# Performance work log

Measured on AMD Instinct MI355X. Metric: run time of the kernel, lower is better.

## Reference

```python
import jax, jax.numpy as jnp
import numpy as np

N_NODES = 100000


def gcn_layer(x, edge_index, W, b):
    # GCNConv: out = D^{-1/2} (A + I) D^{-1/2} (x W) + b
    N = x.shape[0]
    loop = jnp.arange(N, dtype=edge_index.dtype)
    src = jnp.concatenate([edge_index[0], loop])
    dst = jnp.concatenate([edge_index[1], loop])
    deg = jax.ops.segment_sum(jnp.ones_like(src, dtype=x.dtype), dst, num_segments=N)
    dinv = jnp.where(deg > 0, jax.lax.rsqrt(deg), 0.0)
    norm = dinv[src] * dinv[dst]  # [E+N]
    h = x @ W  # [N, out]
    msg = h[src] * norm[:, None]  # [E+N, out]
    out = jax.ops.segment_sum(msg, dst, num_segments=N)
    return out + b


def setup_inputs() -> dict:
    key = jax.random.key(0)
    ks = jax.random.split(key, 8)
    x = jax.random.normal(ks[0], (N_NODES, 128), dtype=jnp.float32)
    edge_index = jax.random.randint(ks[1], (2, 1600000), 0, N_NODES, dtype=jnp.int32)
    def glorot(k, fan_in, fan_out):
        s = jnp.sqrt(6.0 / (fan_in + fan_out)).astype(jnp.float32)
        return jax.random.uniform(k, (fan_in, fan_out), jnp.float32, -s, s)
    return {
        "x": x,
        "edge_index": edge_index,
        "W1": glorot(ks[2], 128, 64), "b1": jnp.zeros((64,), jnp.float32),
        "W2": glorot(ks[3], 64, 128), "b2": jnp.zeros((128,), jnp.float32),
        "W3": glorot(ks[4], 128, 64), "b3": jnp.zeros((64,), jnp.float32),
    }


def reference(x, edge_index, W1, b1, W2, b2, W3, b3):
    h = jax.nn.relu(gcn_layer(x, edge_index, W1, b1))
    h = jax.nn.relu(gcn_layer(h, edge_index, W2, b2))
    out = gcn_layer(h, edge_index, W3, b3)
    return out
```

## Files before the change

kernel.cpp:

```cpp
#include <hip/hip_runtime.h>
#include <hip/hip_fp16.h>
#include <stdint.h>


#define NWGA 256
#define CMAX 8

struct __align__(8) Half4 { __half x, y, z, w; };

__device__ __forceinline__ float4 fma4(float a, float4 b, float4 c) {
  return make_float4(fmaf(a, b.x, c.x), fmaf(a, b.y, c.y),
                     fmaf(a, b.z, c.z), fmaf(a, b.w, c.w));
}

__global__ __launch_bounds__(256) void bucket_hist_kernel(
    const int* __restrict__ dst, int E, int chunk, int NBUK,
    int* __restrict__ M ) {
  __shared__ int hist[512];
  const int w = blockIdx.x, t = threadIdx.x;
  for (int i = t; i < NBUK; i += 256) hist[i] = 0;
  __syncthreads();
  const int e0 = w * chunk;
  const int e1 = min(e0 + chunk, E);
  for (int e = e0 + t; e < e1; e += 256) atomicAdd(&hist[dst[e] >> 8], 1);
  __syncthreads();
  for (int i = t; i < NBUK; i += 256) M[i * NWGA + w] = hist[i];
}

__global__ void scan_blocksum(const int* __restrict__ data, int len,
                              int* __restrict__ bsum) {
  __shared__ int s[256];
  int i = blockIdx.x * 256 + threadIdx.x;
  s[threadIdx.x] = (i < len) ? data[i] : 0;
  __syncthreads();
  for (int off = 128; off > 0; off >>= 1) {
    if (threadIdx.x < off) s[threadIdx.x] += s[threadIdx.x + off];
    __syncthreads();
  }
  if (threadIdx.x == 0) bsum[blockIdx.x] = s[0];
}

__global__ void scan_bsums(int* bsum, int NB) {
  __shared__ int s[512];
  int t = threadIdx.x;
  int v = (t < NB) ? bsum[t] : 0;
  s[t] = v;
  __syncthreads();
  for (int off = 1; off < 512; off <<= 1) {
    int u = (t >= off) ? s[t - off] : 0;
    __syncthreads();
    s[t] += u;
    __syncthreads();
  }
  if (t < NB) bsum[t] = s[t] - v;
}

__global__ void scan_final(int* __restrict__ data, int len,
                           const int* __restrict__ bsum) {
  __shared__ int s[256];
  int t = threadIdx.x;
  int i = blockIdx.x * 256 + t;
  int v = (i < len) ? data[i] : 0;
  s[t] = v;
  __syncthreads();
  for (int off = 1; off < 256; off <<= 1) {
    int u = (t >= off) ? s[t - off] : 0;
    __syncthreads();
    s[t] += u;
    __syncthreads();
  }
  if (i < len) data[i] = bsum[blockIdx.x] + s[t] - v;
}

__global__ __launch_bounds__(256) void bucket_scatter_kernel(
    const int* __restrict__ ei, int E, int chunk, int NBUK,
    const int* __restrict__ Mscan, int2* __restrict__ edata1) {
  __shared__ int cur[512];
  const int w = blockIdx.x, t = threadIdx.x;
  for (int i = t; i < NBUK; i += 256) cur[i] = Mscan[i * NWGA + w];
  __syncthreads();
  const int e0 = w * chunk;
  const int e1 = min(e0 + chunk, E);
  for (int e = e0 + t; e < e1; e += 256) {
    int s = ei[e];
    int d = ei[E + e];
    int pos = atomicAdd(&cur[d >> 8], 1);
    edata1[pos] = make_int2(s, d);
  }
}

__global__ __launch_bounds__(256) void bucket_sort_kernel(
    const int2* __restrict__ edata1, const int* __restrict__ Mscan, int E,
    int N, int NBUK, int* __restrict__ offsets, float* __restrict__ dinv,
    int* __restrict__ edata2) {
  __shared__ int hist[256];
  __shared__ int cursor[256];
  const int b = blockIdx.x, t = threadIdx.x;
  const int ebase = Mscan[b * NWGA];
  const int eend = (b + 1 < NBUK) ? Mscan[(b + 1) * NWGA] : E;
  const int nodebase = b << 8;
  const int node = nodebase + t;
  const int base = ebase + min(nodebase, N);
  hist[t] = (node < N) ? 1 : 0;
  __syncthreads();
  for (int e = ebase + t; e < eend; e += 256)
    atomicAdd(&hist[edata1[e].y - nodebase], 1);
  __syncthreads();
  const int deg = hist[t];
  for (int off = 1; off < 256; off <<= 1) {
    int u = (t >= off) ? hist[t - off] : 0;
    __syncthreads();
    hist[t] += u;
    __syncthreads();
  }
  const int excl = hist[t] - deg;
  cursor[t] = base + excl + 1;
  if (node < N) {
    offsets[node] = base + excl;
    dinv[node] = rsqrtf((float)deg);
    edata2[base + excl] = node;
  }
  if (node == N - 1) offsets[N] = E + N;
  __syncthreads();
  for (int e = ebase + t; e < eend; e += 256) {
    int2 sd = edata1[e];
    int pos = atomicAdd(&cursor[sd.y - nodebase], 1);
    edata2[pos] = sd.x;
  }
}

__global__ __launch_bounds__(256) void edge_weight_kernel(
    const int* __restrict__ edata2, int EN, int* __restrict__ ed3) {
  int stride = gridDim.x * blockDim.x;
  for (int e = blockIdx.x * blockDim.x + threadIdx.x; e < EN; e += stride)
    ed3[e] = edata2[e] << 7;
}

template <int K, int D, bool BR, bool DSCALE, typename InT, typename OutT>
__global__ __launch_bounds__(256) void gemm_kernel(
    const InT* __restrict__ X, const float* __restrict__ W,
    const float* __restrict__ bias, const float* __restrict__ dinv,
    OutT* __restrict__ H, int N) {
  constexpr int CG = D / 4;
  constexpr int TY = 256 / CG;
  constexpr int ROWS = TY * 4;
  __shared__ float Ws[K * D];
  for (int i = threadIdx.x; i < K * D / 4; i += 256)
    reinterpret_cast<float4*>(Ws)[i] = reinterpret_cast<const float4*>(W)[i];
  __syncthreads();

  const int tx = threadIdx.x % CG;
  const int ty = threadIdx.x / CG;
  const int rbase = blockIdx.x * ROWS + ty;

  float4 acc[4];
  int r[4];
#pragma unroll
  for (int i = 0; i < 4; i++) {
    acc[i] = make_float4(0.f, 0.f, 0.f, 0.f);
    int rr = rbase + i * TY;
    r[i] = (rr < N) ? rr : (N - 1);
  }

  for (int k = 0; k < K; k += 4) {
    float4 wv0 = *reinterpret_cast<const float4*>(&Ws[(k + 0) * D + tx * 4]);
    float4 wv1 = *reinterpret_cast<const float4*>(&Ws[(k + 1) * D + tx * 4]);
    float4 wv2 = *reinterpret_cast<const float4*>(&Ws[(k + 2) * D + tx * 4]);
    float4 wv3 = *reinterpret_cast<const float4*>(&Ws[(k + 3) * D + tx * 4]);
#pragma unroll
    for (int i = 0; i < 4; i++) {
      float4 xv;
      if constexpr (sizeof(InT) == 2) {
        Half4 xh = *reinterpret_cast<const Half4*>(&X[(size_t)r[i] * K + k]);
        xv = make_float4(__half2float(xh.x), __half2float(xh.y),
                         __half2float(xh.z), __half2float(xh.w));
      } else {
        xv = *reinterpret_cast<const float4*>(&X[(size_t)r[i] * K + k]);
      }
      acc[i] = fma4(xv.x, wv0, acc[i]);
      acc[i] = fma4(xv.y, wv1, acc[i]);
      acc[i] = fma4(xv.z, wv2, acc[i]);
      acc[i] = fma4(xv.w, wv3, acc[i]);
    }
  }

  float4 bv = make_float4(0.f, 0.f, 0.f, 0.f);
  if (BR) bv = *reinterpret_cast<const float4*>(&bias[tx * 4]);

#pragma unroll
  for (int i = 0; i < 4; i++) {
    int rr = rbase + i * TY;
    if (rr < N) {
      float4 v = acc[i];
      if (BR) {
        v.x = fmaxf(v.x + bv.x, 0.f);
        v.y = fmaxf(v.y + bv.y, 0.f);
        v.z = fmaxf(v.z + bv.z, 0.f);
        v.w = fmaxf(v.w + bv.w, 0.f);
      }
      if (DSCALE) {
        float ds = dinv[rr];
        v.x *= ds; v.y *= ds; v.z *= ds; v.w *= ds;
      }
      if constexpr (sizeof(OutT) == 2) {
        Half4 hv = {__float2half(v.x), __float2half(v.y), __float2half(v.z),
                    __float2half(v.w)};
        *reinterpret_cast<Half4*>(&H[(size_t)rr * D + tx * 4]) = hv;
      } else {
        *reinterpret_cast<float4*>(&H[(size_t)rr * D + tx * 4]) = v;
      }
    }
  }
}

template <bool BIAS, bool RELU, bool SCALE_OUT, typename OutT>
__global__ __launch_bounds__(256) void agg_kernel(
    const __half* __restrict__ h, const int* __restrict__ ed,
    const int* __restrict__ offsets, const float* __restrict__ dinv,
    const float* __restrict__ bias, OutT* __restrict__ out, int N) {
  const int wid = blockIdx.x * 4 + (threadIdx.x >> 6);
  const int na = wid * 8;
  if (na >= N) return;
  const int lane = threadIdx.x & 63;
  const int nrem = min(8, N - na);

  const int off_l = offsets[na + min(lane, nrem)];
  const float dn_l = dinv[na + min(lane, nrem - 1)];
  const int eb0 = __shfl(off_l, 0);
  const int eb1 = __shfl(off_l, nrem);
  float bsv = 0.f;
  if (BIAS) bsv = bias[lane];

  int pe[CMAX];
#pragma unroll
  for (int c = 0; c < CMAX; ++c) {
    int idx = eb0 + c * 64 + lane;
    pe[c] = ed[min(idx, eb1 - 1)];
  }

  const char* hb = (const char*)h;
  float acc = 0.f;
  int cur = 0;
  int bnd = __shfl(off_l, 1);
  float dn = __shfl(dn_l, 0);
  int j = eb0;

#define FLUSH()                                                        \
  {                                                                    \
    float v = acc * dn;                                                \
    if (BIAS) v += bsv;                                                \
    if (RELU) v = fmaxf(v, 0.f);                                       \
    if (SCALE_OUT) v *= dn;                                            \
    if constexpr (sizeof(OutT) == 2)                                   \
      out[(size_t)(na + cur) * 64 + lane] = __float2half(v);           \
    else                                                               \
      out[(size_t)(na + cur) * 64 + lane] = v;                         \
    acc = 0.f;                                                         \
    cur++;                                                             \
    bnd = __shfl(off_l, min(cur + 1, 8));                              \
    dn = __shfl(dn_l, min(cur, 7));                                    \
  }

#pragma unroll
  for (int c = 0; c < CMAX; ++c) {
    if (j < eb1) {
      const int pc = pe[c];
      for (int k = 0; k < 64; k += 8) {
        if (j >= eb1) break;
        int so[8];
        float g[8], wv[8];
#pragma unroll
        for (int i = 0; i < 8; ++i) {
          so[i] = __shfl(pc, k + i);
          wv[i] = (j + i < eb1) ? 1.f : 0.f;
        }
#pragma unroll
        for (int i = 0; i < 8; ++i)
          g[i] = __half2float(
              *(const __half*)(hb + (size_t)(unsigned)so[i] + lane * 2));
#pragma unroll
        for (int i = 0; i < 8; ++i) {
          if (j + i == bnd) FLUSH();
          acc = fmaf(g[i], wv[i], acc);
        }
        j += 8;
      }
    }
  }
  for (; j < eb1; ++j) {
    int so = ed[j];
    float g =
        __half2float(*(const __half*)(hb + (size_t)(unsigned)so + lane * 2));
    if (j == bnd) FLUSH();
    acc += g;
  }
  if (cur < nrem) FLUSH();
#undef FLUSH
}

extern "C" void kernel_launch(void* const* d_in, const int* in_sizes, int n_in,
                              void* d_out, int out_size, void* d_ws,
                              size_t ws_size, hipStream_t stream) {
  const float* x  = (const float*)d_in[0];
  const int*   ei = (const int*)d_in[1];
  const float* W1 = (const float*)d_in[2];
  const float* b1 = (const float*)d_in[3];
  const float* W2 = (const float*)d_in[4];
  const float* b2 = (const float*)d_in[5];
  const float* W3 = (const float*)d_in[6];
  const float* b3 = (const float*)d_in[7];

  const int N = in_sizes[0] / 128;
  const int E = in_sizes[1] / 2;
  const int EN = E + N;
  const int NBUK = (N + 255) >> 8;
  const int MLEN = NBUK * NWGA;
  const int chunk = (E + NWGA - 1) / NWGA;

  char* w = (char*)d_ws;
  int* offsets = (int*)w;      w += (size_t)(N + 2) * 4;
  float* dinv = (float*)w;     w += (size_t)N * 4;
  w = (char*)(((uintptr_t)w + 255) & ~(uintptr_t)255);
  int* edata3 = (int*)w;       w += (size_t)EN * 4;
  w = (char*)(((uintptr_t)w + 255) & ~(uintptr_t)255);
  char* regionA = w;           w += (size_t)N * 64 * 2;
  w = (char*)(((uintptr_t)w + 255) & ~(uintptr_t)255);
  char* regionB = w;           w += (size_t)E * 8;
  w = (char*)(((uintptr_t)w + 255) & ~(uintptr_t)255);
  char* regionC = w;           w += (size_t)N * 128 * 2;

  int* M = (int*)regionA;
  int* bsum = M + MLEN;
  int* edata2 = bsum + 512;
  __half* ht1 = (__half*)regionA;
  int2* edata1 = (int2*)regionB;
  __half* a2 = (__half*)regionB;
  __half* hout1 = (__half*)regionC;
  __half* h2 = (__half*)regionC;

  const int NBS = (MLEN + 255) / 256;
  const int NW = (N + 7) / 8;
  const int AGB = (NW + 3) / 4;

  bucket_hist_kernel<<<NWGA, 256, 0, stream>>>(ei + E, E, chunk, NBUK, M);
  scan_blocksum<<<NBS, 256, 0, stream>>>(M, MLEN, bsum);
  scan_bsums<<<1, 512, 0, stream>>>(bsum, NBS);
  scan_final<<<NBS, 256, 0, stream>>>(M, MLEN, bsum);
  bucket_scatter_kernel<<<NWGA, 256, 0, stream>>>(ei, E, chunk, NBUK, M, edata1);
  bucket_sort_kernel<<<NBUK, 256, 0, stream>>>(edata1, M, E, N, NBUK, offsets,
                                               dinv, edata2);
  edge_weight_kernel<<<1024, 256, 0, stream>>>(edata2, EN, edata3);

  gemm_kernel<128, 64, false, true, float, __half>
      <<<(N + 63) / 64, 256, 0, stream>>>(x, W1, nullptr, dinv, ht1, N);
  agg_kernel<true, true, true, __half><<<AGB, 256, 0, stream>>>(
      ht1, edata3, offsets, dinv, b1, hout1, N);

  agg_kernel<false, false, false, __half><<<AGB, 256, 0, stream>>>(
      hout1, edata3, offsets, dinv, nullptr, a2, N);
  gemm_kernel<64, 128, true, false, __half, __half>
      <<<(N + 31) / 32, 256, 0, stream>>>(a2, W2, b2, nullptr, h2, N);

  gemm_kernel<128, 64, false, true, __half, __half>
      <<<(N + 63) / 64, 256, 0, stream>>>(h2, W3, nullptr, dinv, ht1, N);
  agg_kernel<true, false, false, float><<<AGB, 256, 0, stream>>>(
      ht1, edata3, offsets, dinv, b3, (float*)d_out, N);
}
```

Before: 377.9 us.

## Replace FP32 FMA GEMMs with MFMA f16 matrix-core kernels

Result: faster. 337.7 us (-10.6%).

```diff
diff --git a/kernel.cpp b/kernel.cpp
--- a/kernel.cpp
+++ b/kernel.cpp
@@ -6,12 +6,10 @@
 #define NWGA 256
 #define CMAX 8
 
+typedef _Float16 half8 __attribute__((ext_vector_type(8)));
+typedef float f32x4 __attribute__((ext_vector_type(4)));
+
 struct __align__(8) Half4 { __half x, y, z, w; };
-
-__device__ __forceinline__ float4 fma4(float a, float4 b, float4 c) {
-  return make_float4(fmaf(a, b.x, c.x), fmaf(a, b.y, c.y),
-                     fmaf(a, b.z, c.z), fmaf(a, b.w, c.w));
-}
 
 __global__ __launch_bounds__(256) void bucket_hist_kernel(
     const int* __restrict__ dst, int E, int chunk, int NBUK,
@@ -136,78 +134,96 @@
     ed3[e] = edata2[e] << 7;
 }
 
-template <int K, int D, bool BR, bool DSCALE, typename InT, typename OutT>
-__global__ __launch_bounds__(256) void gemm_kernel(
+template <int K, int D, bool BR, bool DSCALE, typename InT>
+__global__ __launch_bounds__(256) void gemm_mfma(
     const InT* __restrict__ X, const float* __restrict__ W,
     const float* __restrict__ bias, const float* __restrict__ dinv,
-    OutT* __restrict__ H, int N) {
-  constexpr int CG = D / 4;
-  constexpr int TY = 256 / CG;
-  constexpr int ROWS = TY * 4;
-  __shared__ float Ws[K * D];
-  for (int i = threadIdx.x; i < K * D / 4; i += 256)
-    reinterpret_cast<float4*>(Ws)[i] = reinterpret_cast<const float4*>(W)[i];
-  __syncthreads();
-
-  const int tx = threadIdx.x % CG;
-  const int ty = threadIdx.x / CG;
-  const int rbase = blockIdx.x * ROWS + ty;
-
-  float4 acc[4];
-  int r[4];
-#pragma unroll
-  for (int i = 0; i < 4; i++) {
-    acc[i] = make_float4(0.f, 0.f, 0.f, 0.f);
-    int rr = rbase + i * TY;
-    r[i] = (rr < N) ? rr : (N - 1);
-  }
-
-  for (int k = 0; k < K; k += 4) {
-    float4 wv0 = *reinterpret_cast<const float4*>(&Ws[(k + 0) * D + tx * 4]);
-    float4 wv1 = *reinterpret_cast<const float4*>(&Ws[(k + 1) * D + tx * 4]);
-    float4 wv2 = *reinterpret_cast<const float4*>(&Ws[(k + 2) * D + tx * 4]);
-    float4 wv3 = *reinterpret_cast<const float4*>(&Ws[(k + 3) * D + tx * 4]);
-#pragma unroll
-    for (int i = 0; i < 4; i++) {
-      float4 xv;
+    _Float16* __restrict__ H, int N) {
+  __shared__ char lds[2 * K * D];
+  const int t = threadIdx.x;
+  for (int idx = t; idx < K * D; idx += 256) {
+    const int k = idx % K;
+    const int d = idx / K;
+    const _Float16 v = (_Float16)W[k * D + d];
+    const int byte =
+        d * (2 * K) + ((((k >> 3) ^ (d & 7)) << 4) | ((k & 7) << 1));
+    *(_Float16*)(lds + byte) = v;
+  }
+  __syncthreads();
+
+  const int w = t >> 6;
+  const int l = t & 63;
+  const int lrow = l & 15;
+  const int lg = l >> 4;
+  const int r0 = blockIdx.x * 128 + w * 32;
+  if (r0 >= N) return;
+
+  f32x4 acc[2][D / 16];
+#pragma unroll
+  for (int rt = 0; rt < 2; ++rt)
+#pragma unroll
+    for (int c = 0; c < D / 16; ++c) acc[rt][c] = (f32x4){0.f, 0.f, 0.f, 0.f};
+
+  int rA[2];
+  rA[0] = min(r0 + lrow, N - 1);
+  rA[1] = min(r0 + 16 + lrow, N - 1);
+
+#pragma unroll
+  for (int s = 0; s < K / 32; ++s) {
+    half8 a[2];
+#pragma unroll
+    for (int rt = 0; rt < 2; ++rt) {
       if constexpr (sizeof(InT) == 2) {
-        Half4 xh = *reinterpret_cast<const Half4*>(&X[(size_t)r[i] * K + k]);
-        xv = make_float4(__half2float(xh.x), __half2float(xh.y),
-                         __half2float(xh.z), __half2float(xh.w));
+        a[rt] = *reinterpret_cast<const half8*>(
+            (const _Float16*)X + (size_t)rA[rt] * K + s * 32 + lg * 8);
       } else {
-        xv = *reinterpret_cast<const float4*>(&X[(size_t)r[i] * K + k]);
+        const float* xp = (const float*)X + (size_t)rA[rt] * K + s * 32 + lg * 8;
+        float4 lo = *reinterpret_cast<const float4*>(xp);
+        float4 hi = *reinterpret_cast<const float4*>(xp + 4);
+        half8 af;
+        af[0] = (_Float16)lo.x; af[1] = (_Float16)lo.y;
+        af[2] = (_Float16)lo.z; af[3] = (_Float16)lo.w;
+        af[4] = (_Float16)hi.x; af[5] = (_Float16)hi.y;
+        af[6] = (_Float16)hi.z; af[7] = (_Float16)hi.w;
+        a[rt] = af;
       }
-      acc[i] = fma4(xv.x, wv0, acc[i]);
-      acc[i] = fma4(xv.y, wv1, acc[i]);
-      acc[i] = fma4(xv.z, wv2, acc[i]);
-      acc[i] = fma4(xv.w, wv3, acc[i]);
     }
-  }
-
-  float4 bv = make_float4(0.f, 0.f, 0.f, 0.f);
-  if (BR) bv = *reinterpret_cast<const float4*>(&bias[tx * 4]);
-
-#pragma unroll
-  for (int i = 0; i < 4; i++) {
-    int rr = rbase + i * TY;
-    if (rr < N) {
-      float4 v = acc[i];
-      if (BR) {
-        v.x = fmaxf(v.x + bv.x, 0.f);
-        v.y = fmaxf(v.y + bv.y, 0.f);
-        v.z = fmaxf(v.z + bv.z, 0.f);
-        v.w = fmaxf(v.w + bv.w, 0.f);
-      }
-      if (DSCALE) {
-        float ds = dinv[rr];
-        v.x *= ds; v.y *= ds; v.z *= ds; v.w *= ds;
-      }
-      if constexpr (sizeof(OutT) == 2) {
-        Half4 hv = {__float2half(v.x), __float2half(v.y), __float2half(v.z),
-                    __float2half(v.w)};
-        *reinterpret_cast<Half4*>(&H[(size_t)rr * D + tx * 4]) = hv;
-      } else {
-        *reinterpret_cast<float4*>(&H[(size_t)rr * D + tx * 4]) = v;
+    half8 b[D / 16];
+#pragma unroll
+    for (int c = 0; c < D / 16; ++c) {
+      const int d = c * 16 + lrow;
+      const int g = s * 4 + lg;
+      b[c] = *reinterpret_cast<const half8*>(
+          lds + d * (2 * K) + (((g ^ (d & 7)) << 4)));
+    }
+#pragma unroll
+    for (int rt = 0; rt < 2; ++rt)
+#pragma unroll
+      for (int c = 0; c < D / 16; ++c)
+        acc[rt][c] = __builtin_amdgcn_mfma_f32_16x16x32_f16(a[rt], b[c],
+                                                            acc[rt][c], 0, 0, 0);
+  }
+
+  float bv[D / 16];
+  if (BR) {
+#pragma unroll
+    for (int c = 0; c < D / 16; ++c) bv[c] = bias[c * 16 + lrow];
+  }
+#pragma unroll
+  for (int rt = 0; rt < 2; ++rt) {
+#pragma unroll
+    for (int r = 0; r < 4; ++r) {
+      const int row = r0 + rt * 16 + lg * 4 + r;
+      if (row < N) {
+        float ds = 1.f;
+        if (DSCALE) ds = dinv[row];
+#pragma unroll
+        for (int c = 0; c < D / 16; ++c) {
+          float v = acc[rt][c][r];
+          if (BR) v = fmaxf(v + bv[c], 0.f);
+          if (DSCALE) v *= ds;
+          H[(size_t)row * D + c * 16 + lrow] = (_Float16)v;
+        }
       }
     }
   }
@@ -332,15 +348,16 @@
   int* M = (int*)regionA;
   int* bsum = M + MLEN;
   int* edata2 = bsum + 512;
-  __half* ht1 = (__half*)regionA;
+  _Float16* ht1 = (_Float16*)regionA;
   int2* edata1 = (int2*)regionB;
-  __half* a2 = (__half*)regionB;
-  __half* hout1 = (__half*)regionC;
-  __half* h2 = (__half*)regionC;
+  _Float16* a2 = (_Float16*)regionB;
+  _Float16* hout1 = (_Float16*)regionC;
+  _Float16* h2 = (_Float16*)regionC;
 
   const int NBS = (MLEN + 255) / 256;
   const int NW = (N + 7) / 8;
   const int AGB = (NW + 3) / 4;
+  const int GGB = (N + 127) / 128;
 
   bucket_hist_kernel<<<NWGA, 256, 0, stream>>>(ei + E, E, chunk, NBUK, M);
   scan_blocksum<<<NBS, 256, 0, stream>>>(M, MLEN, bsum);
@@ -351,18 +368,18 @@
                                                dinv, edata2);
   edge_weight_kernel<<<1024, 256, 0, stream>>>(edata2, EN, edata3);
 
-  gemm_kernel<128, 64, false, true, float, __half>
-      <<<(N + 63) / 64, 256, 0, stream>>>(x, W1, nullptr, dinv, ht1, N);
+  gemm_mfma<128, 64, false, true, float><<<GGB, 256, 0, stream>>>(
+      x, W1, nullptr, dinv, ht1, N);
   agg_kernel<true, true, true, __half><<<AGB, 256, 0, stream>>>(
-      ht1, edata3, offsets, dinv, b1, hout1, N);
+      (const __half*)ht1, edata3, offsets, dinv, b1, (__half*)hout1, N);
 
   agg_kernel<false, false, false, __half><<<AGB, 256, 0, stream>>>(
-      hout1, edata3, offsets, dinv, nullptr, a2, N);
-  gemm_kernel<64, 128, true, false, __half, __half>
-      <<<(N + 31) / 32, 256, 0, stream>>>(a2, W2, b2, nullptr, h2, N);
-
-  gemm_kernel<128, 64, false, true, __half, __half>
-      <<<(N + 63) / 64, 256, 0, stream>>>(h2, W3, nullptr, dinv, ht1, N);
+      (const __half*)hout1, edata3, offsets, dinv, nullptr, (__half*)a2, N);
+  gemm_mfma<64, 128, true, false, _Float16><<<GGB, 256, 0, stream>>>(
+      a2, W2, b2, nullptr, h2, N);
+
+  gemm_mfma<128, 64, false, true, _Float16><<<GGB, 256, 0, stream>>>(
+      h2, W3, nullptr, dinv, ht1, N);
   agg_kernel<true, false, false, float><<<AGB, 256, 0, stream>>>(
-      ht1, edata3, offsets, dinv, b3, (float*)d_out, N);
-}
+      (const __half*)ht1, edata3, offsets, dinv, b3, (float*)d_out, N);
+}
```
